# Kernel tuning notes

Hardware: AMD Instinct MI355X
Metric: run time of the kernel (lower is better)

Reference implementation:

```python
import jax, jax.numpy as jnp
import numpy as np

B, L, H = 8, 1024, 1024
E, K, I = 8, 2, 256
N_SHARED = 2
IS = I * N_SHARED
NHEADS = 4
HD = H // NHEADS
EPS = 1e-6


def rmsnorm(x, w):
    xf = x.astype(jnp.float32)
    var = jnp.mean(xf * xf, axis=-1, keepdims=True)
    return w * (xf * jax.lax.rsqrt(var + EPS)).astype(x.dtype)


def setup_inputs():
    key = jax.random.key(0)
    ks = jax.random.split(key, 12)
    s = 0.02
    return {
        "hidden_states": jax.random.normal(ks[0], (B, L, H), jnp.float32),
        "true_counts": jax.random.randint(ks[1], (B,), 1, L + 1),
        "context_norm_w": jnp.ones((H,), jnp.float32),
        "in_proj_w": jax.random.normal(ks[2], (3 * H, H), jnp.float32) * s,
        "in_proj_b": jnp.zeros((3 * H,), jnp.float32),
        "out_proj_w": jax.random.normal(ks[3], (H, H), jnp.float32) * s,
        "out_proj_b": jnp.zeros((H,), jnp.float32),
        "gate_norm_w": jnp.ones((H,), jnp.float32),
        "gate_w": jax.random.normal(ks[4], (E, H), jnp.float32) * s,
        "expert_norm_w": jnp.ones((E, H), jnp.float32),
        "expert_gate_w": jax.random.normal(ks[5], (E, I, H), jnp.float32) * s,
        "expert_up_w": jax.random.normal(ks[6], (E, I, H), jnp.float32) * s,
        "expert_down_w": jax.random.normal(ks[7], (E, H, I), jnp.float32) * s,
        "shared_norm_w": jnp.ones((H,), jnp.float32),
        "shared_gate_w": jax.random.normal(ks[8], (IS, H), jnp.float32) * s,
        "shared_up_w": jax.random.normal(ks[9], (IS, H), jnp.float32) * s,
        "shared_down_w": jax.random.normal(ks[10], (H, IS), jnp.float32) * s,
        "out_gate_w": jnp.zeros((1, H), jnp.float32),
        "out_gate_b": jnp.zeros((1,), jnp.float32),
    }


def reference(hidden_states, true_counts, context_norm_w, in_proj_w, in_proj_b,
              out_proj_w, out_proj_b, gate_norm_w, gate_w, expert_norm_w,
              expert_gate_w, expert_up_w, expert_down_w, shared_norm_w,
              shared_gate_w, shared_up_w, shared_down_w, out_gate_w, out_gate_b):
    Bq, Lq, Hq = hidden_states.shape
    pad = jnp.arange(Lq)[None, :] >= true_counts[:, None]  # [B,L] True = padding

    # --- pre-norm self-attention context layer (eval mode: no dropout) ---
    nx = rmsnorm(hidden_states, context_norm_w)
    qkv = nx @ in_proj_w.T + in_proj_b
    q, k, v = jnp.split(qkv, 3, axis=-1)
    def heads(t):
        return t.reshape(Bq, Lq, NHEADS, HD).transpose(0, 2, 1, 3)
    q, k, v = heads(q), heads(k), heads(v)
    att = jnp.einsum('bhqd,bhkd->bhqk', q, k) / np.float32(np.sqrt(HD))
    att = jnp.where(pad[:, None, None, :], jnp.finfo(att.dtype).min, att)
    att = jax.nn.softmax(att, axis=-1)
    ctx = jnp.einsum('bhqk,bhkd->bhqd', att, v).transpose(0, 2, 1, 3).reshape(Bq, Lq, Hq)
    ctx = ctx @ out_proj_w.T + out_proj_b
    x = hidden_states + ctx
    identity = x

    xf = x.reshape(-1, Hq)  # [N,H]
    N = xf.shape[0]

    # --- top-k gating ---
    gscores = jax.nn.softmax(rmsnorm(xf, gate_norm_w) @ gate_w.T, axis=-1)  # [N,E]
    topw, topi = jax.lax.top_k(gscores, K)
    topw = topw / (jnp.sum(topw, axis=-1, keepdims=True) + 1e-20)  # norm_topk_prob
    w_ne = jnp.zeros((N, E), xf.dtype).at[jnp.arange(N)[:, None], topi].set(topw)

    # --- routed experts: each expert has its own RMSNorm; fold the norm weight
    # into the gate/up projections since rms scale of x is expert-independent ---
    xf32 = xf.astype(jnp.float32)
    xhat = xf * jax.lax.rsqrt(jnp.mean(xf32 * xf32, axis=-1, keepdims=True) + EPS)
    wg = expert_gate_w * expert_norm_w[:, None, :]  # [E,I,H]
    wu = expert_up_w * expert_norm_w[:, None, :]
    g = jax.nn.silu(jnp.einsum('nh,eih->nei', xhat, wg))
    u = jnp.einsum('nh,eih->nei', xhat, wu)
    # weighted combine folded into the down projection (linear in the intermediate)
    y = jnp.einsum('nei,ne,ehi->nh', g * u, w_ne, expert_down_w)
    y = y.reshape(Bq, Lq, Hq)

    # --- shared experts ---
    sx = rmsnorm(identity, shared_norm_w)
    y = y + (jax.nn.silu(sx @ shared_gate_w.T) * (sx @ shared_up_w.T)) @ shared_down_w.T

    # --- output gate + padding mask ---
    gate_score = jax.nn.sigmoid(y @ out_gate_w.T + out_gate_b)  # [B,L,1]
    y_gated = y * gate_score
    y_gated = jnp.where(pad[..., None], jnp.zeros((), y.dtype), y_gated)
    return y_gated
```

## Files before the change

kernel.cpp:

```cpp
#include <hip/hip_runtime.h>
#include <hip/hip_bf16.h>

typedef unsigned short u16;
typedef unsigned int   u32;
typedef short bf16x8 __attribute__((ext_vector_type(8)));
typedef float f32x4  __attribute__((ext_vector_type(4)));

#define DEV static __device__ __forceinline__

#define Bc 8
#define Lc 1024
#define Hc 1024
#define Ec 8
#define Ic 256
#define ISc 512
#define NHc 4
#define HDc 256
#define NTOK 8192
#define EPSc 1e-6f
#define MAXSLOTS 17408

DEV u16 f2bf(float f){
  u32 u = __float_as_uint(f);
  return (u16)((u + 0x7fffu + ((u >> 16) & 1u)) >> 16);
}
DEV float bf2f(u16 h){ return __uint_as_float(((u32)h) << 16); }

DEV void gload_lds16(const void* g, void* l){
  __builtin_amdgcn_global_load_lds((const __attribute__((address_space(1))) u32*)g,
                                   (__attribute__((address_space(3))) u32*)l, 16, 0, 0);
}

template<int EPI, int BIAS, int SKIP, int SWZ>
__global__ __launch_bounds__(256)
void gemm3(const u16* __restrict__ Ahi, const u16* __restrict__ Alo,
           const u16* __restrict__ Bhi, const u16* __restrict__ Blo,
           void* __restrict__ Cv, const float* __restrict__ bias,
           const float* __restrict__ Res,
           int M, int N, int K, int lda, int ldb, int ldc,
           long sAin, long sAout, long sBin, long sBout, long sCin, long sCout,
           int loOffC, int biasStride, const int* __restrict__ tc, int bbase)
{
  __shared__ u16 lsAh[128*32];
  __shared__ u16 lsAl[128*32];
  __shared__ u16 lsBh[128*32];
  __shared__ u16 lsBl[128*32];
  int m_i, n_i, z;
  if (SWZ == 1){
    const int NB = gridDim.x*gridDim.y;
    const int L = blockIdx.x + gridDim.x*(blockIdx.y + gridDim.y*blockIdx.z);
    const int r = L & 7, k = L >> 3;
    z = r + 8*(k / NB);
    const int idx = k % NB;
    n_i = idx % gridDim.x; m_i = idx / gridDim.x;
  } else if (SWZ == 2){
    m_i = blockIdx.x; n_i = blockIdx.y; z = blockIdx.z;
  } else {
    n_i = blockIdx.x; m_i = blockIdx.y; z = blockIdx.z;
  }
  const int n0 = n_i*128, m0 = m_i*128;
  const int zin = z & 3, zout = z >> 2;
  if (SKIP == 1){ const int c = tc[bbase + zin]; if (m0 >= c || n0 >= c) return; }
  if (SKIP == 2){ const int c = tc[bbase + zin]; if (m0 >= c) return;
                  const int kl = (c + 31) & ~31; K = K < kl ? K : kl; }
  if (SKIP == 3){ if ((m0 & 1023) >= tc[m0 >> 10]) return; }
  const long aoff = (long)zin*sAin + (long)zout*sAout;
  const long boff = (long)zin*sBin + (long)zout*sBout;
  const long coff = (long)zin*sCin + (long)zout*sCout;
  const u16* Ahb = Ahi + aoff;
  const u16* Alb = Alo + aoff;
  const u16* Bhb = Bhi + boff;
  const u16* Blb = Blo + boff;
  const int t = threadIdx.x, lane = t & 63;
  const int w = t >> 6, wm = w >> 1, wn = w & 1;
  const int fr = lane & 15, kg = lane >> 4;
  const int srow = t >> 2, scol = (t & 3) * 8;
  f32x4 acc[4][4] = {};

  for (int kb = 0; kb < K; kb += 32){
    gload_lds16(Ahb + (long)(m0 +      srow)*lda + kb + scol, &lsAh[srow*32 + scol]);
    gload_lds16(Ahb + (long)(m0 + 64 + srow)*lda + kb + scol, &lsAh[(64+srow)*32 + scol]);
    gload_lds16(Alb + (long)(m0 +      srow)*lda + kb + scol, &lsAl[srow*32 + scol]);
    gload_lds16(Alb + (long)(m0 + 64 + srow)*lda + kb + scol, &lsAl[(64+srow)*32 + scol]);
    gload_lds16(Bhb + (long)(n0 +      srow)*ldb + kb + scol, &lsBh[srow*32 + scol]);
    gload_lds16(Bhb + (long)(n0 + 64 + srow)*ldb + kb + scol, &lsBh[(64+srow)*32 + scol]);
    gload_lds16(Blb + (long)(n0 +      srow)*ldb + kb + scol, &lsBl[srow*32 + scol]);
    gload_lds16(Blb + (long)(n0 + 64 + srow)*ldb + kb + scol, &lsBl[(64+srow)*32 + scol]);
    asm volatile("s_waitcnt vmcnt(0)" ::: "memory");
    __syncthreads();
    bf16x8 ah[4], al[4], bh[4], bl[4];
#pragma unroll
    for (int i = 0; i < 4; i++){
      ah[i] = *(const bf16x8*)&lsAh[(wm*64 + i*16 + fr)*32 + kg*8];
      al[i] = *(const bf16x8*)&lsAl[(wm*64 + i*16 + fr)*32 + kg*8];
      bh[i] = *(const bf16x8*)&lsBh[(wn*64 + i*16 + fr)*32 + kg*8];
      bl[i] = *(const bf16x8*)&lsBl[(wn*64 + i*16 + fr)*32 + kg*8];
    }
#pragma unroll
    for (int mi = 0; mi < 4; mi++)
#pragma unroll
      for (int ni = 0; ni < 4; ni++){
        acc[mi][ni] = __builtin_amdgcn_mfma_f32_16x16x32_bf16(ah[mi], bh[ni], acc[mi][ni], 0, 0, 0);
        acc[mi][ni] = __builtin_amdgcn_mfma_f32_16x16x32_bf16(ah[mi], bl[ni], acc[mi][ni], 0, 0, 0);
        acc[mi][ni] = __builtin_amdgcn_mfma_f32_16x16x32_bf16(al[mi], bh[ni], acc[mi][ni], 0, 0, 0);
      }
    __syncthreads();
  }

  const int r4 = (lane >> 4) * 4;
#pragma unroll
  for (int mi = 0; mi < 4; mi++){
#pragma unroll
    for (int ni = 0; ni < 4; ni++){
      const int col = n0 + wn*64 + ni*16 + fr;
      const float bb = BIAS ? bias[zin*biasStride + col] : 0.f;
#pragma unroll
      for (int r = 0; r < 4; r++){
        const int row = m0 + wm*64 + mi*16 + r4 + r;
        float v = acc[mi][ni][r] + bb;
        if (EPI == 0){
          u16 hv = f2bf(v), lv = f2bf(v - bf2f(hv));
          long idx = coff + (long)row*ldc + col;
          ((u16*)Cv)[idx] = hv;
          ((u16*)Cv)[idx + loOffC] = lv;
        } else if (EPI == 1){
          ((float*)Cv)[coff + (long)row*ldc + col] = v;
        } else if (EPI == 2){
          long idx = coff + (long)row*ldc + col;
          ((float*)Cv)[idx] = v + Res[idx];
        } else {
          u16 hv = f2bf(v), lv = f2bf(v - bf2f(hv));
          int b = row >> 10, q = row & 1023;
          int h = col >> 8, d = col & 255;
          long o = ((long)(b*NHc + h)*HDc + d)*2048 + q;
          ((u16*)Cv)[o] = hv;
          ((u16*)Cv)[o + 1024] = lv;
        }
      }
    }
  }
}

template<int EPI, int SKIP, int SWZ>
__global__ __launch_bounds__(256)
void gemm_bt(const u16* __restrict__ A, const u16* __restrict__ B,
             void* __restrict__ Cv,
             int M, int N, int K, int lda, int ldb, int ldc,
             long sAz, long sBz, long sCz, const int* __restrict__ tc)
{
  __shared__ u16 lsA[128*32];
  __shared__ u16 lsB[128*32];
  int m_i, n_i;
  if (SWZ == 2){ m_i = blockIdx.x; n_i = blockIdx.y; }
  else         { n_i = blockIdx.x; m_i = blockIdx.y; }
  const int z = blockIdx.z;
  const int n0 = n_i*128, m0 = m_i*128;
  if (SKIP == 3){ if ((m0 & 1023) >= tc[m0 >> 10]) return; }
  const u16* Ab = A + (long)z*sAz;
  const u16* Bb = B + (long)z*sBz;
  const int t = threadIdx.x, lane = t & 63;
  const int w = t >> 6, wm = w >> 1, wn = w & 1;
  const int fr = lane & 15, kg = lane >> 4;
  const int srow = t >> 2, scol = (t & 3) * 8;
  f32x4 acc[4][4] = {};

  for (int kb = 0; kb < K; kb += 32){
    gload_lds16(Ab + (long)(m0 +      srow)*lda + kb + scol, &lsA[srow*32 + scol]);
    gload_lds16(Ab + (long)(m0 + 64 + srow)*lda + kb + scol, &lsA[(64+srow)*32 + scol]);
    gload_lds16(Bb + (long)(n0 +      srow)*ldb + kb + scol, &lsB[srow*32 + scol]);
    gload_lds16(Bb + (long)(n0 + 64 + srow)*ldb + kb + scol, &lsB[(64+srow)*32 + scol]);
    asm volatile("s_waitcnt vmcnt(0)" ::: "memory");
    __syncthreads();
    bf16x8 av[4], bv[4];
#pragma unroll
    for (int i = 0; i < 4; i++){
      av[i] = *(const bf16x8*)&lsA[(wm*64 + i*16 + fr)*32 + kg*8];
      bv[i] = *(const bf16x8*)&lsB[(wn*64 + i*16 + fr)*32 + kg*8];
    }
#pragma unroll
    for (int mi = 0; mi < 4; mi++)
#pragma unroll
      for (int ni = 0; ni < 4; ni++)
        acc[mi][ni] = __builtin_amdgcn_mfma_f32_16x16x32_bf16(av[mi], bv[ni], acc[mi][ni], 0, 0, 0);
    __syncthreads();
  }

  const int r4 = (lane >> 4) * 4;
#pragma unroll
  for (int mi = 0; mi < 4; mi++){
#pragma unroll
    for (int ni = 0; ni < 4; ni++){
      const int col = n0 + wn*64 + ni*16 + fr;
#pragma unroll
      for (int r = 0; r < 4; r++){
        const int row = m0 + wm*64 + mi*16 + r4 + r;
        const long idx = (long)z*sCz + (long)row*ldc + col;
        float v = acc[mi][ni][r];
        if      (EPI == 0) ((u16*)Cv)[idx]   = f2bf(v);
        else if (EPI == 1) ((float*)Cv)[idx] = v;
        else               ((float*)Cv)[idx] += v;
      }
    }
  }
}

__global__ __launch_bounds__(256)
void gemm_gu_gather(const u16* __restrict__ A, const u16* __restrict__ Ball,
                    u16* __restrict__ Cg, const int* __restrict__ sidx,
                    const int* __restrict__ counts, const int* __restrict__ offs)
{
  __shared__ u16 lsA[128*32];
  __shared__ u16 lsB[128*32];
  const int e = blockIdx.z;
  const int cnt = counts[e];
  const int obase = offs[e];
  const int padc = offs[e+1] - obase;
  const int m0 = blockIdx.y*128;
  if (m0 >= padc) return;
  const int n0 = blockIdx.x*128;
  const u16* B = Ball + (long)e*512*1024;
  const int t = threadIdx.x, lane = t & 63;
  const int w = t >> 6, wm = w >> 1, wn = w & 1;
  const int fr = lane & 15, kg = lane >> 4;
  const int srow = t >> 2, scol = (t & 3) * 8;
  const int s0 = m0 + srow, s1 = m0 + 64 + srow;
  const int tok0 = (s0 < cnt) ? sidx[e*NTOK + s0] : 0;
  const int tok1 = (s1 < cnt) ? sidx[e*NTOK + s1] : 0;
  f32x4 acc[4][4] = {};

  for (int kb = 0; kb < 1024; kb += 32){
    gload_lds16(A + (long)tok0*1024 + kb + scol, &lsA[srow*32 + scol]);
    gload_lds16(A + (long)tok1*1024 + kb + scol, &lsA[(64+srow)*32 + scol]);
    gload_lds16(B + (long)(n0 +      srow)*1024 + kb + scol, &lsB[srow*32 + scol]);
    gload_lds16(B + (long)(n0 + 64 + srow)*1024 + kb + scol, &lsB[(64+srow)*32 + scol]);
    asm volatile("s_waitcnt vmcnt(0)" ::: "memory");
    __syncthreads();
    bf16x8 av[4], bv[4];
#pragma unroll
    for (int i = 0; i < 4; i++){
      av[i] = *(const bf16x8*)&lsA[(wm*64 + i*16 + fr)*32 + kg*8];
      bv[i] = *(const bf16x8*)&lsB[(wn*64 + i*16 + fr)*32 + kg*8];
    }
#pragma unroll
    for (int mi = 0; mi < 4; mi++)
#pragma unroll
      for (int ni = 0; ni < 4; ni++)
        acc[mi][ni] = __builtin_amdgcn_mfma_f32_16x16x32_bf16(av[mi], bv[ni], acc[mi][ni], 0, 0, 0);
    __syncthreads();
  }

  const int r4 = (lane >> 4) * 4;
#pragma unroll
  for (int mi = 0; mi < 4; mi++){
#pragma unroll
    for (int ni = 0; ni < 4; ni++){
      const int col = wn*64 + ni*16 + fr + n0;
#pragma unroll
      for (int r = 0; r < 4; r++){
        const int row = m0 + wm*64 + mi*16 + r4 + r;
        Cg[(long)(obase + row)*512 + col] = f2bf(acc[mi][ni][r]);
      }
    }
  }
}

__global__ __launch_bounds__(256)
void gemm_down_slots(const u16* __restrict__ Zg, const u16* __restrict__ Wd,
                     u16* __restrict__ D, const int* __restrict__ offs)
{
  __shared__ u16 lsA[128*32];
  __shared__ u16 lsB[128*32];
  const int m0 = blockIdx.y*128;
  if (m0 >= offs[8]) return;
  int e = 0;
#pragma unroll
  for (int i = 0; i < 7; i++) if (m0 >= offs[i+1]) e = i+1;
  const u16* B = Wd + (long)e*1024*256;
  const int n0 = blockIdx.x*128;
  const int t = threadIdx.x, lane = t & 63;
  const int w = t >> 6, wm = w >> 1, wn = w & 1;
  const int fr = lane & 15, kg = lane >> 4;
  const int srow = t >> 2, scol = (t & 3) * 8;
  f32x4 acc[4][4] = {};

  for (int kb = 0; kb < 256; kb += 32){
    gload_lds16(Zg + (long)(m0 +      srow)*256 + kb + scol, &lsA[srow*32 + scol]);
    gload_lds16(Zg + (long)(m0 + 64 + srow)*256 + kb + scol, &lsA[(64+srow)*32 + scol]);
    gload_lds16(B  + (long)(n0 +      srow)*256 + kb + scol, &lsB[srow*32 + scol]);
    gload_lds16(B  + (long)(n0 + 64 + srow)*256 + kb + scol, &lsB[(64+srow)*32 + scol]);
    asm volatile("s_waitcnt vmcnt(0)" ::: "memory");
    __syncthreads();
    bf16x8 av[4], bv[4];
#pragma unroll
    for (int i = 0; i < 4; i++){
      av[i] = *(const bf16x8*)&lsA[(wm*64 + i*16 + fr)*32 + kg*8];
      bv[i] = *(const bf16x8*)&lsB[(wn*64 + i*16 + fr)*32 + kg*8];
    }
#pragma unroll
    for (int mi = 0; mi < 4; mi++)
#pragma unroll
      for (int ni = 0; ni < 4; ni++)
        acc[mi][ni] = __builtin_amdgcn_mfma_f32_16x16x32_bf16(av[mi], bv[ni], acc[mi][ni], 0, 0, 0);
    __syncthreads();
  }

  const int r4 = (lane >> 4) * 4;
#pragma unroll
  for (int mi = 0; mi < 4; mi++){
#pragma unroll
    for (int ni = 0; ni < 4; ni++){
      const int col = n0 + wn*64 + ni*16 + fr;
#pragma unroll
      for (int r = 0; r < 4; r++){
        const int row = m0 + wm*64 + mi*16 + r4 + r;
        D[(long)row*1024 + col] = f2bf(acc[mi][ni][r]);
      }
    }
  }
}

__global__ void cast_bf16_k(const float* __restrict__ in, u16* __restrict__ out, long n){
  long i = (long)blockIdx.x*blockDim.x + threadIdx.x;
  long st = (long)gridDim.x*blockDim.x;
  for (; i < n; i += st) out[i] = f2bf(in[i]);
}

__global__ void split_cast_k(const float* __restrict__ in, u16* __restrict__ hi,
                             u16* __restrict__ lo, long n){
  long i = (long)blockIdx.x*blockDim.x + threadIdx.x;
  long st = (long)gridDim.x*blockDim.x;
  for (; i < n; i += st){
    float v = in[i];
    u16 h = f2bf(v);
    hi[i] = h;
    lo[i] = f2bf(v - bf2f(h));
  }
}

__global__ void fold_expert_k(const float* __restrict__ g, const float* __restrict__ u,
                              const float* __restrict__ nw, u16* __restrict__ gu, long n){
  long i = (long)blockIdx.x*blockDim.x + threadIdx.x;
  long st = (long)gridDim.x*blockDim.x;
  for (; i < n; i += st){
    int h  = (int)(i & (Hc - 1));
    int ii = (int)((i >> 10) & (Ic - 1));
    int e  = (int)(i >> 18);
    float wv = nw[e*Hc + h];
    long o = (long)e*(2*Ic*Hc) + (long)ii*Hc + h;
    gu[o]         = f2bf(g[i]*wv);
    gu[o + Ic*Hc] = f2bf(u[i]*wv);
  }
}

__global__ __launch_bounds__(256)
void rmsnorm_split_k(const float* __restrict__ x, const float* __restrict__ w1,
                     u16* __restrict__ o){
  const int row = blockIdx.x, t = threadIdx.x, lane = t & 63, w = t >> 6;
  float4 v = ((const float4*)(x + (long)row*Hc))[t];
  float ss = v.x*v.x + v.y*v.y + v.z*v.z + v.w*v.w;
  for (int off = 32; off; off >>= 1) ss += __shfl_xor(ss, off);
  __shared__ float red[4];
  if (lane == 0) red[w] = ss;
  __syncthreads();
  float rs = rsqrtf((red[0]+red[1]+red[2]+red[3])*(1.f/Hc) + EPSc);
  float4 wv = ((const float4*)w1)[t];
  float f0 = v.x*rs*wv.x, f1 = v.y*rs*wv.y, f2 = v.z*rs*wv.z, f3 = v.w*rs*wv.w;
  ushort4 hv, lv;
  hv.x = f2bf(f0); lv.x = f2bf(f0 - bf2f(hv.x));
  hv.y = f2bf(f1); lv.y = f2bf(f1 - bf2f(hv.y));
  hv.z = f2bf(f2); lv.z = f2bf(f2 - bf2f(hv.z));
  hv.w = f2bf(f3); lv.w = f2bf(f3 - bf2f(hv.w));
  u16* r16 = o + (long)row*2048;
  ((ushort4*)r16)[t] = hv;
  ((ushort4*)(r16 + 1024))[t] = lv;
}

__global__ __launch_bounds__(256)
void rmsnorm_k(const float* __restrict__ x, u16* __restrict__ o1,
               const float* __restrict__ w2, u16* __restrict__ o2){
  const int row = blockIdx.x, t = threadIdx.x, lane = t & 63, w = t >> 6;
  float4 v = ((const float4*)(x + (long)row*Hc))[t];
  float ss = v.x*v.x + v.y*v.y + v.z*v.z + v.w*v.w;
  for (int off = 32; off; off >>= 1) ss += __shfl_xor(ss, off);
  __shared__ float red[4];
  if (lane == 0) red[w] = ss;
  __syncthreads();
  float rs = rsqrtf((red[0]+red[1]+red[2]+red[3])*(1.f/Hc) + EPSc);
  ushort4 ov;
  ov.x = f2bf(v.x*rs); ov.y = f2bf(v.y*rs); ov.z = f2bf(v.z*rs); ov.w = f2bf(v.w*rs);
  ((ushort4*)o1)[(long)row*256 + t] = ov;
  float4 wv = ((const float4*)w2)[t];
  ov.x = f2bf(v.x*rs*wv.x); ov.y = f2bf(v.y*rs*wv.y);
  ov.z = f2bf(v.z*rs*wv.z); ov.w = f2bf(v.w*rs*wv.w);
  ((ushort4*)o2)[(long)row*256 + t] = ov;
}

__global__ __launch_bounds__(256)
void softmax2_k(float* __restrict__ S, const int* __restrict__ cnt, int bbase){
  const int rid = blockIdx.x;
  const int b = bbase + ((rid >> 10) & 3);
  const int n = cnt[b];
  if ((rid & 1023) >= n) return;
  float* row = S + (long)rid*Lc;
  const int t = threadIdx.x, lane = t & 63, w = t >> 6;
  float4 v = ((const float4*)row)[t];
  const float sc = 0.0625f;
  float vals[4] = {v.x*sc, v.y*sc, v.z*sc, v.w*sc};
  const int c = t*4;
  float m = -3.4e38f;
#pragma unroll
  for (int j = 0; j < 4; j++) if (c + j < n) m = fmaxf(m, vals[j]);
  for (int o = 32; o; o >>= 1) m = fmaxf(m, __shfl_xor(m, o));
  __shared__ float red[8];
  if (lane == 0) red[w] = m;
  __syncthreads();
  m = fmaxf(fmaxf(red[0], red[1]), fmaxf(red[2], red[3]));
  float p[4], s = 0.f;
#pragma unroll
  for (int j = 0; j < 4; j++){ p[j] = (c + j < n) ? __expf(vals[j] - m) : 0.f; s += p[j]; }
  for (int o = 32; o; o >>= 1) s += __shfl_xor(s, o);
  if (lane == 0) red[4 + w] = s;
  __syncthreads();
  const float inv = 1.f / (red[4]+red[5]+red[6]+red[7]);
  ushort4 hv, lv;
  float q0 = p[0]*inv, q1 = p[1]*inv, q2 = p[2]*inv, q3 = p[3]*inv;
  hv.x = f2bf(q0); lv.x = f2bf(q0 - bf2f(hv.x));
  hv.y = f2bf(q1); lv.y = f2bf(q1 - bf2f(hv.y));
  hv.z = f2bf(q2); lv.z = f2bf(q2 - bf2f(hv.z));
  hv.w = f2bf(q3); lv.w = f2bf(q3 - bf2f(hv.w));
  u16* r16 = (u16*)S + (long)rid*2048;
  ((ushort4*)r16)[t] = hv;
  ((ushort4*)(r16 + 1024))[t] = lv;
}

__global__ __launch_bounds__(256)
void gating_score_k(const float* __restrict__ x, const float* __restrict__ gnw,
                    const float* __restrict__ gw, const int* __restrict__ tcnt,
                    int* __restrict__ topi, float* __restrict__ topw){
  const int t = threadIdx.x, lane = t & 63, w = t >> 6;
  const int n = blockIdx.x*4 + w;
  const int b = n >> 10, l = n & 1023;
  if (l >= tcnt[b]) return;
  const float* xr = x + (long)n*Hc;
  float ss = 0.f, sc[8] = {0,0,0,0,0,0,0,0};
  for (int j = 0; j < 16; j++){
    int d = j*64 + lane;
    float xv = xr[d];
    ss += xv*xv;
    float xg = xv * gnw[d];
#pragma unroll
    for (int e = 0; e < 8; e++) sc[e] += xg * gw[e*Hc + d];
  }
  for (int o = 32; o; o >>= 1){
    ss += __shfl_xor(ss, o);
#pragma unroll
    for (int e = 0; e < 8; e++) sc[e] += __shfl_xor(sc[e], o);
  }
  float rs = rsqrtf(ss*(1.f/Hc) + EPSc);
  float m = -3.4e38f;
#pragma unroll
  for (int e = 0; e < 8; e++){ sc[e] *= rs; m = fmaxf(m, sc[e]); }
  float p[8], sum = 0.f;
#pragma unroll
  for (int e = 0; e < 8; e++){ p[e] = __expf(sc[e] - m); sum += p[e]; }
  float inv = 1.f/sum;
#pragma unroll
  for (int e = 0; e < 8; e++) p[e] *= inv;
  int i1 = 0; float v1 = p[0];
#pragma unroll
  for (int e = 1; e < 8; e++) if (p[e] > v1){ v1 = p[e]; i1 = e; }
  int i2 = -1; float v2 = -1.f;
#pragma unroll
  for (int e = 0; e < 8; e++) if (e != i1 && p[e] > v2){ v2 = p[e]; i2 = e; }
  if (lane == 0){
    float dn = v1 + v2 + 1e-20f;
    topi[2*n] = i1; topi[2*n + 1] = i2;
    topw[2*n] = v1/dn; topw[2*n + 1] = v2/dn;
  }
}

__global__ __launch_bounds__(1024)
void route_scan_k(const int* __restrict__ tcnt, const int* __restrict__ topi,
                  const float* __restrict__ topw, int* __restrict__ counts,
                  int* __restrict__ offs, int* __restrict__ sidx,
                  int* __restrict__ gpos, float* __restrict__ wG){
  __shared__ int hist[1024][8];
  __shared__ int soffs[9];
  const int t = threadIdx.x;
  for (int i = t; i < MAXSLOTS; i += 1024) wG[i] = 0.f;
  int h[8] = {0,0,0,0,0,0,0,0};
  const int n0 = t*8;
  int e0[8], e1[8];
#pragma unroll
  for (int k = 0; k < 8; k++){
    const int n = n0 + k;
    const int b = n >> 10, l = n & 1023;
    const bool val = l < tcnt[b];
    e0[k] = val ? topi[2*n]   : -1;
    e1[k] = val ? topi[2*n+1] : -1;
    if (val){ h[e0[k]]++; h[e1[k]]++; }
  }
#pragma unroll
  for (int e = 0; e < 8; e++) hist[t][e] = h[e];
  __syncthreads();
  for (int off = 1; off < 1024; off <<= 1){
    int v[8];
#pragma unroll
    for (int e = 0; e < 8; e++)
      v[e] = hist[t][e] + ((t >= off) ? hist[t - off][e] : 0);
    __syncthreads();
#pragma unroll
    for (int e = 0; e < 8; e++) hist[t][e] = v[e];
    __syncthreads();
  }
  if (t == 0){
    int o = 0; soffs[0] = 0; offs[0] = 0;
    for (int e = 0; e < 8; e++){
      int c = hist[1023][e];
      counts[e] = c;
      o += (c + 127) & ~127;
      soffs[e+1] = o;
      offs[e+1] = o;
    }
  }
  __syncthreads();
  int run[8];
#pragma unroll
  for (int e = 0; e < 8; e++) run[e] = hist[t][e] - h[e];
#pragma unroll
  for (int k = 0; k < 8; k++){
    const int n = n0 + k;
    if (e0[k] >= 0){
      const int p0 = run[e0[k]]++;
      const int p1 = run[e1[k]]++;
      sidx[e0[k]*NTOK + p0] = n;
      sidx[e1[k]*NTOK + p1] = n;
      const int g0 = soffs[e0[k]] + p0, g1 = soffs[e1[k]] + p1;
      gpos[2*n] = g0; gpos[2*n+1] = g1;
      wG[g0] = topw[2*n]; wG[g1] = topw[2*n+1];
    } else {
      gpos[2*n] = 0; gpos[2*n+1] = 0;
    }
  }
}

__global__ void act_shared_k(const u16* __restrict__ gu, u16* __restrict__ z, long n){
  long i = (long)blockIdx.x*blockDim.x + threadIdx.x;
  long st = (long)gridDim.x*blockDim.x;
  for (; i < n; i += st){
    long nn = i >> 9;
    int  ii = (int)(i & (ISc - 1));
    float gv = bf2f(gu[nn*1024 + ii]);
    float uv = bf2f(gu[nn*1024 + ISc + ii]);
    z[i] = f2bf(gv/(1.f + __expf(-gv)) * uv);
  }
}

__global__ void act_slots_k(const u16* __restrict__ gu, const float* __restrict__ wG,
                            const int* __restrict__ offs, u16* __restrict__ z){
  long nmax = (long)offs[8]*256;
  long st = (long)gridDim.x*blockDim.x;
  for (long i = (long)blockIdx.x*blockDim.x + threadIdx.x; i < nmax; i += st){
    long s = i >> 8;
    int ii = (int)(i & 255);
    float gv = bf2f(gu[s*512 + ii]);
    float uv = bf2f(gu[s*512 + 256 + ii]);
    z[i] = f2bf(gv/(1.f + __expf(-gv)) * uv * wG[s]);
  }
}

__global__ void act_expert_k(const u16* __restrict__ gu, const int* __restrict__ topi,
                             const float* __restrict__ topw, int e,
                             u16* __restrict__ z, long n){
  long i = (long)blockIdx.x*blockDim.x + threadIdx.x;
  long st = (long)gridDim.x*blockDim.x;
  for (; i < n; i += st){
    long nn = i >> 8;
    int  ii = (int)(i & (Ic - 1));
    float wv = 0.f;
    if      (topi[2*nn]     == e) wv = topw[2*nn];
    else if (topi[2*nn + 1] == e) wv = topw[2*nn + 1];
    float gv = bf2f(gu[nn*512 + ii]);
    float uv = bf2f(gu[nn*512 + Ic + ii]);
    z[i] = f2bf(gv/(1.f + __expf(-gv)) * uv * wv);
  }
}

__global__ __launch_bounds__(256)
void final2_k(const float* __restrict__ ysh, const u16* __restrict__ D,
              const int* __restrict__ gpos, const float* __restrict__ ogw,
              const float* __restrict__ ogb, const int* __restrict__ cnt,
              float* __restrict__ out){
  const int t = threadIdx.x, lane = t & 63, w = t >> 6;
  const int n = blockIdx.x*4 + w;
  const int b = n >> 10, l = n & 1023;
  float* outr = out + (long)n*Hc;
  if (l >= cnt[b]){
#pragma unroll
    for (int j = 0; j < 16; j++) outr[j*64 + lane] = 0.f;
    return;
  }
  const float* yr = ysh + (long)n*Hc;
  const u16* d0 = D + (long)gpos[2*n]*1024;
  const u16* d1 = D + (long)gpos[2*n+1]*1024;
  float dot = 0.f, yv[16];
#pragma unroll
  for (int j = 0; j < 16; j++){
    int d = j*64 + lane;
    yv[j] = yr[d] + bf2f(d0[d]) + bf2f(d1[d]);
    dot += yv[j]*ogw[d];
  }
  for (int o = 32; o; o >>= 1) dot += __shfl_xor(dot, o);
  float s = 1.f/(1.f + __expf(-(dot + ogb[0])));
#pragma unroll
  for (int j = 0; j < 16; j++) outr[j*64 + lane] = yv[j]*s;
}

__global__ __launch_bounds__(256)
void final_k(const float* __restrict__ y, const float* __restrict__ ogw,
             const float* __restrict__ ogb, const int* __restrict__ cnt,
             float* __restrict__ out){
  const int t = threadIdx.x, lane = t & 63, w = t >> 6;
  const int n = blockIdx.x*4 + w;
  const int b = n >> 10, l = n & 1023;
  const bool pad = l >= cnt[b];
  const float* yr = y + (long)n*Hc;
  float dot = 0.f, yv[16];
#pragma unroll
  for (int j = 0; j < 16; j++){
    int d = j*64 + lane;
    yv[j] = yr[d];
    dot += yv[j]*ogw[d];
  }
  for (int o = 32; o; o >>= 1) dot += __shfl_xor(dot, o);
  float s = 1.f/(1.f + __expf(-(dot + ogb[0])));
  float* outr = out + (long)n*Hc;
#pragma unroll
  for (int j = 0; j < 16; j++){
    int d = j*64 + lane;
    outr[d] = pad ? 0.f : yv[j]*s;
  }
}

__global__ void sentinel_k(float* out){ out[0] = 1.0e9f; }

extern "C" void kernel_launch(void* const* d_in, const int* in_sizes, int n_in,
                              void* d_out, int out_size, void* d_ws, size_t ws_size,
                              hipStream_t stream){
  const float* hidden  = (const float*)d_in[0];
  const int*   cnt     = (const int*)  d_in[1];
  const float* ctx_nw  = (const float*)d_in[2];
  const float* Wqkv    = (const float*)d_in[3];
  const float* in_b    = (const float*)d_in[4];
  const float* Woutp   = (const float*)d_in[5];
  const float* out_b   = (const float*)d_in[6];
  const float* gate_nw = (const float*)d_in[7];
  const float* gate_w  = (const float*)d_in[8];
  const float* exp_nw  = (const float*)d_in[9];
  const float* Weg     = (const float*)d_in[10];
  const float* Weu     = (const float*)d_in[11];
  const float* Wed     = (const float*)d_in[12];
  const float* sh_nw   = (const float*)d_in[13];
  const float* Wsg     = (const float*)d_in[14];
  const float* Wsu     = (const float*)d_in[15];
  const float* Wsd     = (const float*)d_in[16];
  const float* ogw     = (const float*)d_in[17];
  const float* ogb     = (const float*)d_in[18];
  float* out = (float*)d_out;

  const size_t MB = 1024*1024;
  char* ws = (char*)d_ws;
  size_t off = 0;
  auto alloc = [&](size_t bytes)->char*{
    char* p = ws + off; off += (bytes + 255) & ~(size_t)255; return p;
  };
  u16* wWqH  = (u16*)alloc((size_t)3072*1024*2);
  u16* wWqL  = (u16*)alloc((size_t)3072*1024*2);
  u16* wWoH  = (u16*)alloc((size_t)1024*1024*2);
  u16* wWoL  = (u16*)alloc((size_t)1024*1024*2);
  u16* wWgu  = (u16*)alloc((size_t)Ec*2*Ic*Hc*2);
  u16* wWd   = (u16*)alloc((size_t)Ec*Hc*Ic*2);
  u16* wWsgu = (u16*)alloc((size_t)2*ISc*Hc*2);
  u16* wWsd  = (u16*)alloc((size_t)Hc*ISc*2);
  int*   wTopI = (int*)  alloc((size_t)NTOK*2*4);
  float* wTopW = (float*)alloc((size_t)NTOK*2*4);
  int*   wGpos = (int*)  alloc((size_t)NTOK*2*4);
  int*   wSidx = (int*)  alloc((size_t)Ec*NTOK*4);
  float* wG    = (float*)alloc((size_t)MAXSLOTS*4);
  int*   wCnts = (int*)  alloc(64);
  int*   wOffs = (int*)  alloc(64);
  char* P1 = alloc(32*MB);
  char* P2 = alloc(32*MB);
  char* P3 = alloc(32*MB);
  char* P4 = alloc(32*MB);
  size_t fixed = off;
  const bool big = (fixed + 64*MB) <= ws_size;
  char* P5 = alloc(big ? 64*MB : 16*MB);
  if (off > ws_size){ sentinel_k<<<1,1,0,stream>>>(out); return; }

  u16*   wNx   = (u16*)P1;
  u16*   wCtx  = (u16*)P1;
  float* wY    = (float*)P1;
  u16*   wQp   = (u16*)P2;
  u16*   wXhat = (u16*)P2;
  u16*   wSx   = (u16*)(P2 + 16*MB);
  u16*   wKp   = (u16*)P3;
  float* wX    = (float*)P3;
  u16*   wGUg  = (u16*)P3;
  u16*   wZg   = (u16*)(P3 + 18*MB);
  u16*   wGUe  = (u16*)P3;
  u16*   wZe   = (u16*)(P3 + 8*MB);
  u16*   wVtp  = (u16*)P4;
  u16*   wGUs  = (u16*)P4;
  u16*   wZs   = (u16*)(P4 + 16*MB);
  float* wS    = (float*)P5;
  u16*   wD    = (u16*)P5;

  split_cast_k<<<4096, 256, 0, stream>>>(Wqkv,  wWqH, wWqL, (long)3072*1024);
  split_cast_k<<<2048, 256, 0, stream>>>(Woutp, wWoH, wWoL, (long)1024*1024);
  cast_bf16_k<<<2048, 256, 0, stream>>>(Wed, wWd, (long)Ec*Hc*Ic);
  cast_bf16_k<<<1024, 256, 0, stream>>>(Wsg, wWsgu,                (long)ISc*Hc);
  cast_bf16_k<<<1024, 256, 0, stream>>>(Wsu, wWsgu + (long)ISc*Hc, (long)ISc*Hc);
  cast_bf16_k<<<1024, 256, 0, stream>>>(Wsd, wWsd, (long)Hc*ISc);
  fold_expert_k<<<2048, 256, 0, stream>>>(Weg, Weu, exp_nw, wWgu, (long)Ec*Ic*Hc);

  rmsnorm_split_k<<<NTOK, 256, 0, stream>>>(hidden, ctx_nw, wNx);
  if (big){
    gemm3<0, 1, 3, 2><<<dim3(64, 8, 2), 256, 0, stream>>>(
        wNx, wNx + 1024, wWqH, wWqL, wQp, in_b, nullptr,
        NTOK, 1024, 1024, 2048, 1024, 2048,
        0, 0, (long)1024*1024, 0, (long)16*1024*1024, 0,
        1024, 1024, cnt, 0);
    gemm3<3, 1, 3, 2><<<dim3(64, 8, 1), 256, 0, stream>>>(
        wNx, wNx + 1024, wWqH + (long)2048*1024, wWqL + (long)2048*1024, wVtp,
        in_b + 2048, nullptr, NTOK, 1024, 1024, 2048, 1024, 0,
        0, 0, 0, 0, 0, 0, 0, 0, cnt, 0);
  } else {
    gemm3<0, 1, 0, 0><<<dim3(8, 64, 2), 256, 0, stream>>>(
        wNx, wNx + 1024, wWqH, wWqL, wQp, in_b, nullptr,
        NTOK, 1024, 1024, 2048, 1024, 2048,
        0, 0, (long)1024*1024, 0, (long)16*1024*1024, 0,
        1024, 1024, nullptr, 0);
    gemm3<3, 1, 0, 0><<<dim3(8, 64, 1), 256, 0, stream>>>(
        wNx, wNx + 1024, wWqH + (long)2048*1024, wWqL + (long)2048*1024, wVtp,
        in_b + 2048, nullptr, NTOK, 1024, 1024, 2048, 1024, 0,
        0, 0, 0, 0, 0, 0, 0, 0, nullptr, 0);
  }

  if (big){
    for (int g = 0; g < 2; g++){
      const int bbase = g*4;
      const long tokoff = (long)g*4*Lc*2048;
      const u16* Qb = wQp + tokoff;
      const u16* Kb = wKp + tokoff;
      gemm3<1, 0, 1, 1><<<dim3(8, 8, 16), 256, 0, stream>>>(
          Qb, Qb + 1024, Kb, Kb + 1024, wS, nullptr, nullptr,
          Lc, Lc, HDc, 2048, 2048, Lc,
          (long)Lc*2048, (long)HDc,
          (long)Lc*2048, (long)HDc,
          (long)Lc*Lc,   (long)4*Lc*Lc,
          0, 0, cnt, bbase);
      softmax2_k<<<16*1024, 256, 0, stream>>>(wS, cnt, bbase);
      const u16* Vb = wVtp + (long)g*4*NHc*HDc*2048;
      u16* Cb = wCtx + tokoff;
      gemm3<0, 0, 2, 1><<<dim3(2, 8, 16), 256, 0, stream>>>(
          (const u16*)wS, (const u16*)wS + 1024, Vb, Vb + 1024, Cb, nullptr, nullptr,
          Lc, HDc, Lc, 2048, 2048, 2048,
          (long)Lc*2048,     (long)4*Lc*2048,
          (long)NHc*HDc*2048,(long)HDc*2048,
          (long)Lc*2048,     (long)HDc,
          1024, 0, cnt, bbase);
    }
  } else {
    for (int g = 0; g < 8; g++){
      const int hf = g >> 2, hbase = g & 3, bbase = hf*4;
      const long tokoff = (long)hf*4*Lc*2048;
      const u16* Qb = wQp + tokoff + hbase*HDc;
      const u16* Kb = wKp + tokoff + hbase*HDc;
      gemm3<1, 0, 1, 0><<<dim3(8, 8, 4), 256, 0, stream>>>(
          Qb, Qb + 1024, Kb, Kb + 1024, wS, nullptr, nullptr,
          Lc, Lc, HDc, 2048, 2048, Lc,
          (long)Lc*2048, (long)HDc,
          (long)Lc*2048, (long)HDc,
          (long)Lc*Lc,   (long)4*Lc*Lc,
          0, 0, cnt, bbase);
      softmax2_k<<<4*1024, 256, 0, stream>>>(wS, cnt, bbase);
      const u16* Vb = wVtp + (long)hf*4*NHc*HDc*2048 + (long)hbase*HDc*2048;
      u16* Cb = wCtx + tokoff + hbase*HDc;
      gemm3<0, 0, 2, 0><<<dim3(2, 8, 4), 256, 0, stream>>>(
          (const u16*)wS, (const u16*)wS + 1024, Vb, Vb + 1024, Cb, nullptr, nullptr,
          Lc, HDc, Lc, 2048, 2048, 2048,
          (long)Lc*2048,     (long)4*Lc*2048,
          (long)NHc*HDc*2048,(long)HDc*2048,
          (long)Lc*2048,     (long)HDc,
          1024, 0, cnt, bbase);
    }
  }

  if (big){
    gemm3<2, 1, 3, 2><<<dim3(64, 8, 1), 256, 0, stream>>>(
        wCtx, wCtx + 1024, wWoH, wWoL, wX, out_b, hidden,
        NTOK, 1024, 1024, 2048, 1024, 1024,
        0, 0, 0, 0, 0, 0, 0, 0, cnt, 0);
  } else {
    gemm3<2, 1, 0, 0><<<dim3(8, 64, 1), 256, 0, stream>>>(
        wCtx, wCtx + 1024, wWoH, wWoL, wX, out_b, hidden,
        NTOK, 1024, 1024, 2048, 1024, 1024,
        0, 0, 0, 0, 0, 0, 0, 0, nullptr, 0);
  }

  gating_score_k<<<NTOK/4, 256, 0, stream>>>(wX, gate_nw, gate_w, cnt, wTopI, wTopW);
  route_scan_k<<<1, 1024, 0, stream>>>(cnt, wTopI, wTopW, wCnts, wOffs,
                                       wSidx, wGpos, wG);
  rmsnorm_k<<<NTOK, 256, 0, stream>>>(wX, wXhat, sh_nw, wSx);

  if (big){
    gemm_bt<0, 3, 2><<<dim3(64, 8, 1), 256, 0, stream>>>(
        wSx, wWsgu, wGUs, NTOK, 2*ISc, 1024, 1024, 1024, 2*ISc, 0, 0, 0, cnt);
    act_shared_k<<<4096, 256, 0, stream>>>(wGUs, wZs, (long)NTOK*ISc);
    gemm_bt<1, 3, 2><<<dim3(64, 8, 1), 256, 0, stream>>>(
        wZs, wWsd, wY, NTOK, 1024, ISc, ISc, ISc, 1024, 0, 0, 0, cnt);
  } else {
    gemm_bt<0, 0, 0><<<dim3(8, 64, 1), 256, 0, stream>>>(
        wSx, wWsgu, wGUs, NTOK, 2*ISc, 1024, 1024, 1024, 2*ISc, 0, 0, 0, nullptr);
    act_shared_k<<<4096, 256, 0, stream>>>(wGUs, wZs, (long)NTOK*ISc);
    gemm_bt<1, 0, 0><<<dim3(8, 64, 1), 256, 0, stream>>>(
        wZs, wWsd, wY, NTOK, 1024, ISc, ISc, ISc, 1024, 0, 0, 0, nullptr);
  }

  if (big){
    gemm_gu_gather<<<dim3(4, 64, Ec), 256, 0, stream>>>(
        wXhat, wWgu, wGUg, wSidx, wCnts, wOffs);
    act_slots_k<<<2048, 256, 0, stream>>>(wGUg, wG, wOffs, wZg);
    gemm_down_slots<<<dim3(8, MAXSLOTS/128, 1), 256, 0, stream>>>(
        wZg, wWd, wD, wOffs);
    final2_k<<<NTOK/4, 256, 0, stream>>>(wY, wD, wGpos, ogw, ogb, cnt, out);
  } else {
    for (int e = 0; e < Ec; e++){
      gemm_bt<0, 0, 0><<<dim3(4, 64, 1), 256, 0, stream>>>(
          wXhat, wWgu + (long)e*2*Ic*Hc, wGUe, NTOK, 2*Ic, 1024, 1024, 1024, 2*Ic,
          0, 0, 0, nullptr);
      act_expert_k<<<2048, 256, 0, stream>>>(wGUe, wTopI, wTopW, e, wZe, (long)NTOK*Ic);
      gemm_bt<2, 0, 0><<<dim3(8, 64, 1), 256, 0, stream>>>(
          wZe, wWd + (long)e*Hc*Ic, wY, NTOK, 1024, Ic, Ic, Ic, 1024, 0, 0, 0, nullptr);
    }
    final_k<<<NTOK/4, 256, 0, stream>>>(wY, ogw, ogb, cnt, out);
  }
}
```

Measured before the change: 659.8 us.

## Fuse QKV projection launches, batch attention over all batches, merge norm and gating

Merges the separate QK and V projection GEMMs into one three-slice launch whose epilogue writes Q/K row-major and V transposed. When the workspace is large enough, runs the score GEMM, softmax and context GEMM once over all 8 batches instead of two groups of 4. The gating-score kernel is folded into the RMSNorm kernel so the hidden row is read once. Tile skipping by token count is now always on. The trade-offs are a larger workspace requirement for the fully batched path and a more complex epilogue branch.

```diff
diff --git a/kernel.cpp b/kernel.cpp
--- a/kernel.cpp
+++ b/kernel.cpp
@@ -31,7 +31,7 @@
                                    (__attribute__((address_space(3))) u32*)l, 16, 0, 0);
 }
 
-template<int EPI, int BIAS, int SKIP, int SWZ>
+template<int EPI, int BIAS, int SKIP, int SWZ, int ZDEC>
 __global__ __launch_bounds__(256)
 void gemm3(const u16* __restrict__ Ahi, const u16* __restrict__ Alo,
            const u16* __restrict__ Bhi, const u16* __restrict__ Blo,
@@ -59,7 +59,8 @@
     n_i = blockIdx.x; m_i = blockIdx.y; z = blockIdx.z;
   }
   const int n0 = n_i*128, m0 = m_i*128;
-  const int zin = z & 3, zout = z >> 2;
+  const int zin  = ZDEC ? (z & 7)  : (z & 3);
+  const int zout = ZDEC ? (z >> 3) : (z >> 2);
   if (SKIP == 1){ const int c = tc[bbase + zin]; if (m0 >= c || n0 >= c) return; }
   if (SKIP == 2){ const int c = tc[bbase + zin]; if (m0 >= c) return;
                   const int kl = (c + 31) & ~31; K = K < kl ? K : kl; }
@@ -128,13 +129,26 @@
         } else if (EPI == 2){
           long idx = coff + (long)row*ldc + col;
           ((float*)Cv)[idx] = v + Res[idx];
-        } else {
+        } else if (EPI == 3){
           u16 hv = f2bf(v), lv = f2bf(v - bf2f(hv));
           int b = row >> 10, q = row & 1023;
           int h = col >> 8, d = col & 255;
           long o = ((long)(b*NHc + h)*HDc + d)*2048 + q;
           ((u16*)Cv)[o] = hv;
           ((u16*)Cv)[o + 1024] = lv;
+        } else {
+          u16 hv = f2bf(v), lv = f2bf(v - bf2f(hv));
+          if (z < 2){
+            long idx = (long)z*sCin + (long)row*ldc + col;
+            ((u16*)Cv)[idx] = hv;
+            ((u16*)Cv)[idx + loOffC] = lv;
+          } else {
+            int b = row >> 10, q = row & 1023;
+            int h = col >> 8, d = col & 255;
+            long o = sCout + ((long)(b*NHc + h)*HDc + d)*2048 + q;
+            ((u16*)Cv)[o] = hv;
+            ((u16*)Cv)[o + 1024] = lv;
+          }
         }
       }
     }
@@ -376,29 +390,76 @@
 }
 
 __global__ __launch_bounds__(256)
-void rmsnorm_k(const float* __restrict__ x, u16* __restrict__ o1,
-               const float* __restrict__ w2, u16* __restrict__ o2){
+void norm_gate_k(const float* __restrict__ x, const float* __restrict__ shw,
+                 const float* __restrict__ gnw, const float* __restrict__ gw,
+                 const int* __restrict__ tcnt,
+                 u16* __restrict__ xhat, u16* __restrict__ sx,
+                 int* __restrict__ topi, float* __restrict__ topw){
   const int row = blockIdx.x, t = threadIdx.x, lane = t & 63, w = t >> 6;
   float4 v = ((const float4*)(x + (long)row*Hc))[t];
   float ss = v.x*v.x + v.y*v.y + v.z*v.z + v.w*v.w;
   for (int off = 32; off; off >>= 1) ss += __shfl_xor(ss, off);
   __shared__ float red[4];
+  __shared__ float gred[4][8];
   if (lane == 0) red[w] = ss;
   __syncthreads();
   float rs = rsqrtf((red[0]+red[1]+red[2]+red[3])*(1.f/Hc) + EPSc);
   ushort4 ov;
   ov.x = f2bf(v.x*rs); ov.y = f2bf(v.y*rs); ov.z = f2bf(v.z*rs); ov.w = f2bf(v.w*rs);
-  ((ushort4*)o1)[(long)row*256 + t] = ov;
-  float4 wv = ((const float4*)w2)[t];
-  ov.x = f2bf(v.x*rs*wv.x); ov.y = f2bf(v.y*rs*wv.y);
-  ov.z = f2bf(v.z*rs*wv.z); ov.w = f2bf(v.w*rs*wv.w);
-  ((ushort4*)o2)[(long)row*256 + t] = ov;
+  ((ushort4*)xhat)[(long)row*256 + t] = ov;
+  float4 sv = ((const float4*)shw)[t];
+  ov.x = f2bf(v.x*rs*sv.x); ov.y = f2bf(v.y*rs*sv.y);
+  ov.z = f2bf(v.z*rs*sv.z); ov.w = f2bf(v.w*rs*sv.w);
+  ((ushort4*)sx)[(long)row*256 + t] = ov;
+
+  const int b = row >> 10, l = row & 1023;
+  if (l >= tcnt[b]) return;
+  float4 g = ((const float4*)gnw)[t];
+  float xg0 = v.x*g.x, xg1 = v.y*g.y, xg2 = v.z*g.z, xg3 = v.w*g.w;
+  float pe[8];
+#pragma unroll
+  for (int e = 0; e < 8; e++){
+    float4 ww = ((const float4*)(gw + (long)e*Hc))[t];
+    pe[e] = xg0*ww.x + xg1*ww.y + xg2*ww.z + xg3*ww.w;
+  }
+  for (int off = 32; off; off >>= 1){
+#pragma unroll
+    for (int e = 0; e < 8; e++) pe[e] += __shfl_xor(pe[e], off);
+  }
+  if (lane == 0){
+#pragma unroll
+    for (int e = 0; e < 8; e++) gred[w][e] = pe[e];
+  }
+  __syncthreads();
+  if (t == 0){
+    float sc[8], m = -3.4e38f;
+#pragma unroll
+    for (int e = 0; e < 8; e++){
+      sc[e] = (gred[0][e]+gred[1][e]+gred[2][e]+gred[3][e])*rs;
+      m = fmaxf(m, sc[e]);
+    }
+    float p[8], sum = 0.f;
+#pragma unroll
+    for (int e = 0; e < 8; e++){ p[e] = __expf(sc[e] - m); sum += p[e]; }
+    float inv = 1.f/sum;
+#pragma unroll
+    for (int e = 0; e < 8; e++) p[e] *= inv;
+    int i1 = 0; float v1 = p[0];
+#pragma unroll
+    for (int e = 1; e < 8; e++) if (p[e] > v1){ v1 = p[e]; i1 = e; }
+    int i2 = -1; float v2 = -1.f;
+#pragma unroll
+    for (int e = 0; e < 8; e++) if (e != i1 && p[e] > v2){ v2 = p[e]; i2 = e; }
+    float dn = v1 + v2 + 1e-20f;
+    topi[2*row] = i1; topi[2*row + 1] = i2;
+    topw[2*row] = v1/dn; topw[2*row + 1] = v2/dn;
+  }
 }
 
 __global__ __launch_bounds__(256)
-void softmax2_k(float* __restrict__ S, const int* __restrict__ cnt, int bbase){
+void softmax2_k(float* __restrict__ S, const int* __restrict__ cnt, int bbase, int bmask){
   const int rid = blockIdx.x;
-  const int b = bbase + ((rid >> 10) & 3);
+  const int b = bbase + ((rid >> 10) & bmask);
   const int n = cnt[b];
   if ((rid & 1023) >= n) return;
   float* row = S + (long)rid*Lc;
@@ -431,52 +492,6 @@
   u16* r16 = (u16*)S + (long)rid*2048;
   ((ushort4*)r16)[t] = hv;
   ((ushort4*)(r16 + 1024))[t] = lv;
-}
-
-__global__ __launch_bounds__(256)
-void gating_score_k(const float* __restrict__ x, const float* __restrict__ gnw,
-                    const float* __restrict__ gw, const int* __restrict__ tcnt,
-                    int* __restrict__ topi, float* __restrict__ topw){
-  const int t = threadIdx.x, lane = t & 63, w = t >> 6;
-  const int n = blockIdx.x*4 + w;
-  const int b = n >> 10, l = n & 1023;
-  if (l >= tcnt[b]) return;
-  const float* xr = x + (long)n*Hc;
-  float ss = 0.f, sc[8] = {0,0,0,0,0,0,0,0};
-  for (int j = 0; j < 16; j++){
-    int d = j*64 + lane;
-    float xv = xr[d];
-    ss += xv*xv;
-    float xg = xv * gnw[d];
-#pragma unroll
-    for (int e = 0; e < 8; e++) sc[e] += xg * gw[e*Hc + d];
-  }
-  for (int o = 32; o; o >>= 1){
-    ss += __shfl_xor(ss, o);
-#pragma unroll
-    for (int e = 0; e < 8; e++) sc[e] += __shfl_xor(sc[e], o);
-  }
-  float rs = rsqrtf(ss*(1.f/Hc) + EPSc);
-  float m = -3.4e38f;
-#pragma unroll
-  for (int e = 0; e < 8; e++){ sc[e] *= rs; m = fmaxf(m, sc[e]); }
-  float p[8], sum = 0.f;
-#pragma unroll
-  for (int e = 0; e < 8; e++){ p[e] = __expf(sc[e] - m); sum += p[e]; }
-  float inv = 1.f/sum;
-#pragma unroll
-  for (int e = 0; e < 8; e++) p[e] *= inv;
-  int i1 = 0; float v1 = p[0];
-#pragma unroll
-  for (int e = 1; e < 8; e++) if (p[e] > v1){ v1 = p[e]; i1 = e; }
-  int i2 = -1; float v2 = -1.f;
-#pragma unroll
-  for (int e = 0; e < 8; e++) if (e != i1 && p[e] > v2){ v2 = p[e]; i2 = e; }
-  if (lane == 0){
-    float dn = v1 + v2 + 1e-20f;
-    topi[2*n] = i1; topi[2*n + 1] = i2;
-    topw[2*n] = v1/dn; topw[2*n + 1] = v2/dn;
-  }
 }
 
 __global__ __launch_bounds__(1024)
@@ -694,8 +709,9 @@
   char* P3 = alloc(32*MB);
   char* P4 = alloc(32*MB);
   size_t fixed = off;
-  const bool big = (fixed + 64*MB) <= ws_size;
-  char* P5 = alloc(big ? 64*MB : 16*MB);
+  const int mode = (fixed + 128*MB <= ws_size) ? 2 :
+                   (fixed + 64*MB  <= ws_size) ? 1 : 0;
+  char* P5 = alloc(mode == 2 ? 128*MB : mode == 1 ? 64*MB : 16*MB);
   if (off > ws_size){ sentinel_k<<<1,1,0,stream>>>(out); return; }
 
   u16*   wNx   = (u16*)P1;
@@ -725,45 +741,48 @@
   fold_expert_k<<<2048, 256, 0, stream>>>(Weg, Weu, exp_nw, wWgu, (long)Ec*Ic*Hc);
 
   rmsnorm_split_k<<<NTOK, 256, 0, stream>>>(hidden, ctx_nw, wNx);
-  if (big){
-    gemm3<0, 1, 3, 2><<<dim3(64, 8, 2), 256, 0, stream>>>(
-        wNx, wNx + 1024, wWqH, wWqL, wQp, in_b, nullptr,
-        NTOK, 1024, 1024, 2048, 1024, 2048,
-        0, 0, (long)1024*1024, 0, (long)16*1024*1024, 0,
-        1024, 1024, cnt, 0);
-    gemm3<3, 1, 3, 2><<<dim3(64, 8, 1), 256, 0, stream>>>(
-        wNx, wNx + 1024, wWqH + (long)2048*1024, wWqL + (long)2048*1024, wVtp,
-        in_b + 2048, nullptr, NTOK, 1024, 1024, 2048, 1024, 0,
-        0, 0, 0, 0, 0, 0, 0, 0, cnt, 0);
-  } else {
-    gemm3<0, 1, 0, 0><<<dim3(8, 64, 2), 256, 0, stream>>>(
-        wNx, wNx + 1024, wWqH, wWqL, wQp, in_b, nullptr,
-        NTOK, 1024, 1024, 2048, 1024, 2048,
-        0, 0, (long)1024*1024, 0, (long)16*1024*1024, 0,
-        1024, 1024, nullptr, 0);
-    gemm3<3, 1, 0, 0><<<dim3(8, 64, 1), 256, 0, stream>>>(
-        wNx, wNx + 1024, wWqH + (long)2048*1024, wWqL + (long)2048*1024, wVtp,
-        in_b + 2048, nullptr, NTOK, 1024, 1024, 2048, 1024, 0,
-        0, 0, 0, 0, 0, 0, 0, 0, nullptr, 0);
-  }
-
-  if (big){
+  gemm3<4, 1, 3, 2, 0><<<dim3(64, 8, 3), 256, 0, stream>>>(
+      wNx, wNx + 1024, wWqH, wWqL, wQp, in_b, nullptr,
+      NTOK, 1024, 1024, 2048, 1024, 2048,
+      0, 0, (long)1024*1024, 0,
+      (long)16*1024*1024,
+      (long)32*1024*1024,
+      1024, 1024, cnt, 0);
+
+  if (mode == 2){
+    gemm3<1, 0, 1, 1, 1><<<dim3(8, 8, 32), 256, 0, stream>>>(
+        wQp, wQp + 1024, wKp, wKp + 1024, wS, nullptr, nullptr,
+        Lc, Lc, HDc, 2048, 2048, Lc,
+        (long)Lc*2048, (long)HDc,
+        (long)Lc*2048, (long)HDc,
+        (long)Lc*Lc,   (long)8*Lc*Lc,
+        0, 0, cnt, 0);
+    softmax2_k<<<32*1024, 256, 0, stream>>>(wS, cnt, 0, 7);
+    gemm3<0, 0, 2, 1, 1><<<dim3(2, 8, 32), 256, 0, stream>>>(
+        (const u16*)wS, (const u16*)wS + 1024, wVtp, wVtp + 1024, wCtx,
+        nullptr, nullptr,
+        Lc, HDc, Lc, 2048, 2048, 2048,
+        (long)Lc*2048,      (long)8*Lc*2048,
+        (long)NHc*HDc*2048, (long)HDc*2048,
+        (long)Lc*2048,      (long)HDc,
+        1024, 0, cnt, 0);
+  } else if (mode == 1){
     for (int g = 0; g < 2; g++){
       const int bbase = g*4;
       const long tokoff = (long)g*4*Lc*2048;
       const u16* Qb = wQp + tokoff;
       const u16* Kb = wKp + tokoff;
-      gemm3<1, 0, 1, 1><<<dim3(8, 8, 16), 256, 0, stream>>>(
+      gemm3<1, 0, 1, 1, 0><<<dim3(8, 8, 16), 256, 0, stream>>>(
           Qb, Qb + 1024, Kb, Kb + 1024, wS, nullptr, nullptr,
           Lc, Lc, HDc, 2048, 2048, Lc,
           (long)Lc*2048, (long)HDc,
           (long)Lc*2048, (long)HDc,
           (long)Lc*Lc,   (long)4*Lc*Lc,
           0, 0, cnt, bbase);
-      softmax2_k<<<16*1024, 256, 0, stream>>>(wS, cnt, bbase);
+      softmax2_k<<<16*1024, 256, 0, stream>>>(wS, cnt, bbase, 3);
       const u16* Vb = wVtp + (long)g*4*NHc*HDc*2048;
       u16* Cb = wCtx + tokoff;
-      gemm3<0, 0, 2, 1><<<dim3(2, 8, 16), 256, 0, stream>>>(
+      gemm3<0, 0, 2, 1, 0><<<dim3(2, 8, 16), 256, 0, stream>>>(
           (const u16*)wS, (const u16*)wS + 1024, Vb, Vb + 1024, Cb, nullptr, nullptr,
           Lc, HDc, Lc, 2048, 2048, 2048,
           (long)Lc*2048,     (long)4*Lc*2048,
@@ -777,17 +796,17 @@
       const long tokoff = (long)hf*4*Lc*2048;
       const u16* Qb = wQp + tokoff + hbase*HDc;
       const u16* Kb = wKp + tokoff + hbase*HDc;
-      gemm3<1, 0, 1, 0><<<dim3(8, 8, 4), 256, 0, stream>>>(
+      gemm3<1, 0, 1, 0, 0><<<dim3(8, 8, 4), 256, 0, stream>>>(
           Qb, Qb + 1024, Kb, Kb + 1024, wS, nullptr, nullptr,
           Lc, Lc, HDc, 2048, 2048, Lc,
           (long)Lc*2048, (long)HDc,
           (long)Lc*2048, (long)HDc,
           (long)Lc*Lc,   (long)4*Lc*Lc,
           0, 0, cnt, bbase);
-      softmax2_k<<<4*1024, 256, 0, stream>>>(wS, cnt, bbase);
+      softmax2_k<<<4*1024, 256, 0, stream>>>(wS, cnt, bbase, 3);
       const u16* Vb = wVtp + (long)hf*4*NHc*HDc*2048 + (long)hbase*HDc*2048;
       u16* Cb = wCtx + tokoff + hbase*HDc;
-      gemm3<0, 0, 2, 0><<<dim3(2, 8, 4), 256, 0, stream>>>(
+      gemm3<0, 0, 2, 0, 0><<<dim3(2, 8, 4), 256, 0, stream>>>(
           (const u16*)wS, (const u16*)wS + 1024, Vb, Vb + 1024, Cb, nullptr, nullptr,
           Lc, HDc, Lc, 2048, 2048, 2048,
           (long)Lc*2048,     (long)4*Lc*2048,
@@ -797,38 +816,23 @@
     }
   }
 
-  if (big){
-    gemm3<2, 1, 3, 2><<<dim3(64, 8, 1), 256, 0, stream>>>(
-        wCtx, wCtx + 1024, wWoH, wWoL, wX, out_b, hidden,
-        NTOK, 1024, 1024, 2048, 1024, 1024,
-        0, 0, 0, 0, 0, 0, 0, 0, cnt, 0);
-  } else {
-    gemm3<2, 1, 0, 0><<<dim3(8, 64, 1), 256, 0, stream>>>(
-        wCtx, wCtx + 1024, wWoH, wWoL, wX, out_b, hidden,
-        NTOK, 1024, 1024, 2048, 1024, 1024,
-        0, 0, 0, 0, 0, 0, 0, 0, nullptr, 0);
-  }
-
-  gating_score_k<<<NTOK/4, 256, 0, stream>>>(wX, gate_nw, gate_w, cnt, wTopI, wTopW);
+  gemm3<2, 1, 3, 2, 0><<<dim3(64, 8, 1), 256, 0, stream>>>(
+      wCtx, wCtx + 1024, wWoH, wWoL, wX, out_b, hidden,
+      NTOK, 1024, 1024, 2048, 1024, 1024,
+      0, 0, 0, 0, 0, 0, 0, 0, cnt, 0);
+
+  norm_gate_k<<<NTOK, 256, 0, stream>>>(wX, sh_nw, gate_nw, gate_w, cnt,
+                                        wXhat, wSx, wTopI, wTopW);
   route_scan_k<<<1, 1024, 0, stream>>>(cnt, wTopI, wTopW, wCnts, wOffs,
                                        wSidx, wGpos, wG);
-  rmsnorm_k<<<NTOK, 256, 0, stream>>>(wX, wXhat, sh_nw, wSx);
-
-  if (big){
-    gemm_bt<0, 3, 2><<<dim3(64, 8, 1), 256, 0, stream>>>(
-        wSx, wWsgu, wGUs, NTOK, 2*ISc, 1024, 1024, 1024, 2*ISc, 0, 0, 0, cnt);
-    act_shared_k<<<4096, 256, 0, stream>>>(wGUs, wZs, (long)NTOK*ISc);
-    gemm_bt<1, 3, 2><<<dim3(64, 8, 1), 256, 0, stream>>>(
-        wZs, wWsd, wY, NTOK, 1024, ISc, ISc, ISc, 1024, 0, 0, 0, cnt);
-  } else {
-    gemm_bt<0, 0, 0><<<dim3(8, 64, 1), 256, 0, stream>>>(
-        wSx, wWsgu, wGUs, NTOK, 2*ISc, 1024, 1024, 1024, 2*ISc, 0, 0, 0, nullptr);
-    act_shared_k<<<4096, 256, 0, stream>>>(wGUs, wZs, (long)NTOK*ISc);
-    gemm_bt<1, 0, 0><<<dim3(8, 64, 1), 256, 0, stream>>>(
-        wZs, wWsd, wY, NTOK, 1024, ISc, ISc, ISc, 1024, 0, 0, 0, nullptr);
-  }
-
-  if (big){
+
+  gemm_bt<0, 3, 2><<<dim3(64, 8, 1), 256, 0, stream>>>(
+      wSx, wWsgu, wGUs, NTOK, 2*ISc, 1024, 1024, 1024, 2*ISc, 0, 0, 0, cnt);
+  act_shared_k<<<4096, 256, 0, stream>>>(wGUs, wZs, (long)NTOK*ISc);
+  gemm_bt<1, 3, 2><<<dim3(64, 8, 1), 256, 0, stream>>>(
+      wZs, wWsd, wY, NTOK, 1024, ISc, ISc, ISc, 1024, 0, 0, 0, cnt);
+
+  if (mode >= 1){
     gemm_gu_gather<<<dim3(4, 64, Ec), 256, 0, stream>>>(
         wXhat, wWgu, wGUg, wSidx, wCnts, wOffs);
     act_slots_k<<<2048, 256, 0, stream>>>(wGUg, wG, wOffs, wZg);
```

Result: slower. 675.1 us (+2.3%).
